# Performance work log

Hardware: AMD Instinct MI355X
Metric: run time of the kernel (lower is better)

Reference implementation:

```python
import jax, jax.numpy as jnp
import numpy as np


def setup_inputs() -> dict:
    key = jax.random.key(0)
    k0, k1, k2, k3 = jax.random.split(key, 4)
    N, C, H, W, s = 2, 16, 96, 96, 2
    x = jax.random.normal(k0, (N, C, H, W), dtype=jnp.float32)
    pos_mat = jax.random.uniform(k1, (1, H * s * W * s, 3), dtype=jnp.float32)
    mask = jnp.ones((1, 1, H * s, W * s), dtype=bool)
    w1 = jax.random.normal(k2, (3, 256), dtype=jnp.float32) * 0.1
    b1 = jnp.zeros((256,), dtype=jnp.float32)
    w2 = jax.random.normal(k3, (256, 9 * C * C), dtype=jnp.float32) * 0.02
    b2 = jnp.zeros((9 * C * C,), dtype=jnp.float32)
    return {"x": x, "pos_mat": pos_mat, "mask": mask, "w1": w1, "b1": b1,
            "w2": w2, "b2": b2, "r": 2, "hr0": H * s, "hr1": W * s}


def _unfold3x3(x):
    # torch F.unfold(x, kernel_size=3, padding=1) -> [N, C*9, H*W],
    # channel ordering: c slowest, then (kh, kw).
    N, C, H, W = x.shape
    xp = jnp.pad(x, ((0, 0), (0, 0), (1, 1), (1, 1)))
    patches = jnp.stack([xp[:, :, i:i + H, j:j + W]
                         for i in range(3) for j in range(3)], axis=2)  # [N,C,9,H,W]
    return patches.reshape(N, C * 9, H * W)


def reference(x, pos_mat, mask, w1, b1, w2, b2, r, hr0, hr1):
    s = int(np.ceil(r))  # scale_int
    N, C, H, W = x.shape

    # Pos2Weight hypernetwork: Linear(3,256) -> LeakyReLU(0.2) -> Linear(256, 9*C*C)
    p = pos_mat.reshape(-1, 3)                       # [H*s*W*s, 3]
    h = p @ w1 + b1
    h = jnp.where(h >= 0, h, 0.2 * h)
    lw = h @ w2 + b2                                 # [H*s*W*s, 9*C*C]

    # local_weight -> (s^2, H*W, 9C, C)
    lw = lw.reshape(H, s, W, s, 9 * C, C).transpose(1, 3, 0, 2, 4, 5)
    lw = lw.reshape(s * s, H * W, 9 * C, C)

    # repeat_x tiles x s^2 times along batch; all copies are identical, so the
    # unfold of up_x equals the unfold of x broadcast over the s^2 axis.
    cols = _unfold3x3(x).transpose(0, 2, 1)          # [N, H*W, 9C]

    # per-pixel batched matmul: (N,1,HW,1,9C) @ (s^2,HW,9C,C)
    out = jnp.einsum('npk,qpkc->nqpc', cols, lw)     # [N, s^2, H*W, C]

    # (N,s,s,H,W,C) -> (N,C,H,s,W,s) -> (N,C,sH,sW)
    out = out.reshape(N, s, s, H, W, C).transpose(0, 5, 3, 1, 4, 2)
    out = out.reshape(N, C, s * H, s * W)

    # masked_select with an all-True broadcast mask followed by reshape to
    # (N, C, hr0, hr1); with integer scale, hr == (sH, sW) and this is identity.
    re_sr = jnp.reshape(out, (N, C, hr0, hr1))
    return re_sr
```

## Files before the change

kernel.cpp:

```cpp
#include <hip/hip_runtime.h>
#include <stdint.h>

typedef __attribute__((ext_vector_type(8))) short          s16x8;
typedef __attribute__((ext_vector_type(8))) unsigned short u16x8;
typedef __attribute__((ext_vector_type(4))) float          f32x4;

#define HWPIX 9216
#define OSTR  68
#define ABLK  10240

static __device__ __forceinline__ unsigned short f2bf(float f) {
  unsigned int u = __float_as_uint(f);
  u += 0x7fffu + ((u >> 16) & 1u);
  return (unsigned short)(u >> 16);
}

__global__ __launch_bounds__(256)
void ml_prep(const float* __restrict__ x, const float* __restrict__ w2,
             const float* __restrict__ b2,
             unsigned short* __restrict__ Afrag, unsigned short* __restrict__ Bfrag)
{
  int idx = blockIdx.x * 256 + threadIdx.x;
  if (idx < 368640) {
    int bx = idx / 1280, r = idx - bx * 1280;
    int ks = r >> 8, mi = (r >> 6) & 3, lane = r & 63;
    int row = bx * 64 + mi * 16 + (lane & 15);
    int p = row >> 1, n2 = row & 1;
    int hh = p / 96, ww = p - hh * 96;
    int k0 = ks * 32 + (lane >> 4) * 8;
    u16x8 v;
#pragma unroll
    for (int t = 0; t < 8; t++) {
      int k = k0 + t;
      float xv = 0.f;
      if (k < 144) {
        int cc = k / 9, kidx = k - cc * 9;
        int ih = hh + kidx / 3 - 1, iw = ww + (kidx % 3) - 1;
        if (ih >= 0 && ih < 96 && iw >= 0 && iw < 96)
          xv = x[((n2 * 16 + cc) * 96 + ih) * 96 + iw];
      }
      v[t] = f2bf(xv);
    }
    *(u16x8*)(Afrag + (size_t)idx * 8) = v;
    return;
  }
  idx -= 368640;
  if (idx < 87040) {
    int lane = idx & 63;
    int u  = idx >> 6;
    int ni = u & 3;
    int u2 = u >> 2;
    int wid = u2 & 3;
    int u3 = u2 >> 2;
    int ks = u3 % 5;
    int jb = u3 / 5;
    int col = jb * 256 + wid * 64 + ni * 16 + (lane & 15);
    int k0 = ks * 32 + (lane >> 4) * 8;
    u16x8 v;
    if (col < 4096) {
      int j = col >> 4, c = col & 15;
#pragma unroll
      for (int t = 0; t < 8; t++) {
        int k = k0 + t;
        v[t] = (k < 144) ? f2bf(w2[j * 2304 + k * 16 + c]) : (unsigned short)0;
      }
    } else {
      int m = col - 4096;
      int jl = m >> 4, c = m & 15;
#pragma unroll
      for (int t = 0; t < 8; t++) {
        int k = k0 + t;
        v[t] = (jl == 0 && k < 144) ? f2bf(b2[k * 16 + c]) : (unsigned short)0;
      }
    }
    *(u16x8*)(Bfrag + (size_t)idx * 8) = v;
  }
}

struct SmemT {
  unsigned short A[ABLK];
  float hbuf[2][2][32 * OSTR];
};

__global__ __launch_bounds__(512, 2)
void ml_main(const unsigned short* __restrict__ Afrag,
             const unsigned short* __restrict__ Bfrag,
             const float* __restrict__ pos, const float* __restrict__ w1,
             const float* __restrict__ b1,
             float* __restrict__ out)
{
  __shared__ SmemT sm;
  const int tid  = threadIdx.x;
  const int lane = tid & 63;
  const int wid  = tid >> 6;
  const int wni  = wid & 3;
  const int wjb  = wid >> 2;
  const int bx   = blockIdx.x;
  const int p0   = bx * 32;

  const unsigned short* bwv = Bfrag + wni * 2048 + lane * 8;

  const unsigned short* Ablk = Afrag + (size_t)bx * ABLK;
  u16x8 av[3];
#pragma unroll
  for (int i = 0; i < 3; i++) {
    int aid = i * 512 + tid;
    if (aid < 1280) av[i] = *(const u16x8*)(Ablk + aid * 8);
  }

  float pv[4][3];
  {
    int p = p0 + (tid >> 4);
    int hh = p / 96, ww = p - hh * 96;
#pragma unroll
    for (int q = 0; q < 4; q++) {
      int m = hh * 384 + (q >> 1) * 192 + ww * 2 + (q & 1);
      pv[q][0] = pos[m * 3 + 0];
      pv[q][1] = pos[m * 3 + 1];
      pv[q][2] = pos[m * 3 + 2];
    }
  }

#pragma unroll
  for (int i = 0; i < 3; i++) {
    int aid = i * 512 + tid;
    if (aid < 1280) *(u16x8*)(sm.A + aid * 8) = av[i];
  }

  s16x8 br0[4], br1[4];
  {
    const unsigned short* bb = bwv + wjb * 5 * 8192;
#pragma unroll
    for (int ni = 0; ni < 4; ni++)
      br0[ni] = *(const s16x8*)(bb + ni * 512);
  }

  f32x4 oa[4][4];
#pragma unroll
  for (int mi = 0; mi < 4; mi++)
#pragma unroll
    for (int reg = 0; reg < 4; reg++) {
      f32x4 z = {0.f, 0.f, 0.f, 0.f};
      oa[mi][reg] = z;
    }

  __syncthreads();

  auto step = [&](int s, s16x8 (&bx0)[4], s16x8 (&bx1)[4]) {
    {
      int p_h = tid >> 4, jl = tid & 15;
#pragma unroll
      for (int wj = 0; wj < 2; wj++) {
        int jb = 2 * s + wj;
        if (jb <= 16) {
          f32x4 hv;
          if (jb < 16) {
            int j = jb * 16 + jl;
            float wa = w1[j], wb = w1[256 + j], wc = w1[512 + j], bb = b1[j];
#pragma unroll
            for (int q = 0; q < 4; q++) {
              float h = pv[q][0] * wa + pv[q][1] * wb + pv[q][2] * wc + bb;
              hv[q] = (h >= 0.f) ? h : 0.2f * h;
            }
          } else {
            float v = (jl == 0) ? 1.f : 0.f;
            hv[0] = v; hv[1] = v; hv[2] = v; hv[3] = v;
          }
          *(f32x4*)&sm.hbuf[s & 1][wj][p_h * OSTR + jl * 4] = hv;
        }
      }
    }
    __syncthreads();

    const int jb_w = 2 * s + wjb;
    if (jb_w <= 16) {
      f32x4 acc[4][4];
#pragma unroll
      for (int mi = 0; mi < 4; mi++)
#pragma unroll
        for (int ni = 0; ni < 4; ni++) {
          f32x4 z = {0.f, 0.f, 0.f, 0.f};
          acc[mi][ni] = z;
        }

#pragma unroll
      for (int ks = 0; ks < 5; ks++) {
        s16x8 (&bcur)[4]  = (ks & 1) ? bx1 : bx0;
        s16x8 (&bnext)[4] = (ks & 1) ? bx0 : bx1;
        if (ks < 4 || jb_w + 2 <= 16) {
          int njb = (ks < 4) ? jb_w : jb_w + 2;
          int nks = (ks < 4) ? ks + 1 : 0;
          const unsigned short* bb = bwv + (njb * 5 + nks) * 8192;
#pragma unroll
          for (int ni = 0; ni < 4; ni++)
            bnext[ni] = *(const s16x8*)(bb + ni * 512);
        }
        s16x8 af[4];
#pragma unroll
        for (int mi = 0; mi < 4; mi++)
          af[mi] = *(const s16x8*)(sm.A + (ks * 4 + mi) * 512 + lane * 8);
#pragma unroll
        for (int mi = 0; mi < 4; mi++)
#pragma unroll
          for (int ni = 0; ni < 4; ni++)
            acc[mi][ni] = __builtin_amdgcn_mfma_f32_16x16x32_bf16(af[mi], bcur[ni], acc[mi][ni], 0, 0, 0);
      }

      const float* hb = &sm.hbuf[s & 1][wjb][0];
#pragma unroll
      for (int mi = 0; mi < 4; mi++) {
        int pb = mi * 8 + (lane >> 4) * 2;
#pragma unroll
        for (int ni = 0; ni < 4; ni++) {
          int jl = wni * 4 + ni;
          const float* hp = &hb[pb * OSTR + jl * 4];
          f32x4 h0 = *(const f32x4*)hp;
          f32x4 h1 = *(const f32x4*)(hp + OSTR);
          f32x4 a = acc[mi][ni];
          oa[mi][0] += h0 * a[0];
          oa[mi][1] += h0 * a[1];
          oa[mi][2] += h1 * a[2];
          oa[mi][3] += h1 * a[3];
        }
      }
    }
  };

#pragma unroll 1
  for (int s2 = 0; s2 < 4; s2++) {
    step(2 * s2,     br0, br1);
    step(2 * s2 + 1, br1, br0);
  }
  step(8, br0, br1);

  float* outr  = (float*)sm.A;
  float* outr2 = (float*)&sm.hbuf[0][0][0];
  __syncthreads();
  if (wid == 0 || wid == 4) {
    float* dst = (wid == 0) ? outr : outr2;
#pragma unroll
    for (int mi = 0; mi < 4; mi++)
#pragma unroll
      for (int reg = 0; reg < 4; reg++) {
        int row = mi * 16 + (lane >> 4) * 4 + reg;
        *(f32x4*)&dst[row * OSTR + (lane & 15) * 4] = oa[mi][reg];
      }
  }
  __syncthreads();
#pragma unroll 1
  for (int r = 1; r < 4; r++) {
    if (wid == r || wid == r + 4) {
      float* dst = (wid == r) ? outr : outr2;
#pragma unroll
      for (int mi = 0; mi < 4; mi++)
#pragma unroll
        for (int reg = 0; reg < 4; reg++) {
          int row = mi * 16 + (lane >> 4) * 4 + reg;
          f32x4* d = (f32x4*)&dst[row * OSTR + (lane & 15) * 4];
          *d += oa[mi][reg];
        }
    }
    __syncthreads();
  }

  const int hh0 = bx / 3;
  const int ww0 = (bx - hh0 * 3) * 32;
#pragma unroll 1
  for (int i = 0; i < 8; i++) {
    int flat = i * 512 + tid;
    int xl = flat & 63;
    int si = (flat >> 6) & 1;
    int c  = (flat >> 7) & 15;
    int n2 = flat >> 11;
    int pl = xl >> 1, sj = xl & 1;
    int q = si * 2 + sj;
    int row = pl * 2 + n2;
    int idx = row * OSTR + c * 4 + q;
    float v = outr[idx] + outr2[idx];
    out[((n2 * 16 + c) * 192 + hh0 * 2 + si) * 192 + ww0 * 2 + xl] = v;
  }
}

extern "C" void kernel_launch(void* const* d_in, const int* in_sizes, int n_in,
                              void* d_out, int out_size, void* d_ws, size_t ws_size,
                              hipStream_t stream) {
  const float* x   = (const float*)d_in[0];
  const float* pos = (const float*)d_in[1];
  const float* w1  = (const float*)d_in[3];
  const float* b1  = (const float*)d_in[4];
  const float* w2  = (const float*)d_in[5];
  const float* b2  = (const float*)d_in[6];
  float* out = (float*)d_out;

  unsigned short* Afrag = (unsigned short*)d_ws;
  unsigned short* Bfrag = Afrag + (size_t)288 * ABLK;

  ml_prep<<<1780, 256, 0, stream>>>(x, w2, b2, Afrag, Bfrag);
  ml_main<<<288, 512, 0, stream>>>(Afrag, Bfrag, pos, w1, b1, out);
}
```

Baseline: 84.13 us.

## Retile main kernel to 36 pixels per block over 256 blocks with swizzled LDS A

Changes each block from 32 to 36 pixels (72 GEMM rows padded to 80, 5 M-fragments), so the grid becomes 256 blocks, matching the CU count for a single wave. The prep kernel pads A fragments with zero rows, and a second set of position values covers pixels 32..35 for the hidden-layer buffer. It also XOR-swizzles the A fragment layout in shared memory to reduce bank conflicts. In exchange it adds padded MFMA work (80 rows, only 72 used), more registers per thread that may hurt the 2-blocks occupancy, and output stores that no longer cover contiguous row segments.

```diff
diff --git a/kernel.cpp b/kernel.cpp
--- a/kernel.cpp
+++ b/kernel.cpp
@@ -7,7 +7,7 @@
 
 #define HWPIX 9216
 #define OSTR  68
-#define ABLK  10240
+#define ABLK  12800
 
 static __device__ __forceinline__ unsigned short f2bf(float f) {
   unsigned int u = __float_as_uint(f);
@@ -21,30 +21,37 @@
              unsigned short* __restrict__ Afrag, unsigned short* __restrict__ Bfrag)
 {
   int idx = blockIdx.x * 256 + threadIdx.x;
-  if (idx < 368640) {
-    int bx = idx / 1280, r = idx - bx * 1280;
-    int ks = r >> 8, mi = (r >> 6) & 3, lane = r & 63;
-    int row = bx * 64 + mi * 16 + (lane & 15);
-    int p = row >> 1, n2 = row & 1;
-    int hh = p / 96, ww = p - hh * 96;
-    int k0 = ks * 32 + (lane >> 4) * 8;
+  if (idx < 409600) {
+    int bx = idx / 1600, r = idx - bx * 1600;
+    int ks = r / 320, r2 = r - ks * 320;
+    int mi = r2 >> 6, lane = r2 & 63;
+    int rowloc = mi * 16 + (lane & 15);
     u16x8 v;
-#pragma unroll
-    for (int t = 0; t < 8; t++) {
-      int k = k0 + t;
-      float xv = 0.f;
-      if (k < 144) {
-        int cc = k / 9, kidx = k - cc * 9;
-        int ih = hh + kidx / 3 - 1, iw = ww + (kidx % 3) - 1;
-        if (ih >= 0 && ih < 96 && iw >= 0 && iw < 96)
-          xv = x[((n2 * 16 + cc) * 96 + ih) * 96 + iw];
-      }
-      v[t] = f2bf(xv);
+    if (rowloc < 72) {
+      int g = bx * 72 + rowloc;
+      int p = g >> 1, n2 = g & 1;
+      int hh = p / 96, ww = p - hh * 96;
+      int k0 = ks * 32 + (lane >> 4) * 8;
+#pragma unroll
+      for (int t = 0; t < 8; t++) {
+        int k = k0 + t;
+        float xv = 0.f;
+        if (k < 144) {
+          int cc = k / 9, kidx = k - cc * 9;
+          int ih = hh + kidx / 3 - 1, iw = ww + (kidx % 3) - 1;
+          if (ih >= 0 && ih < 96 && iw >= 0 && iw < 96)
+            xv = x[((n2 * 16 + cc) * 96 + ih) * 96 + iw];
+        }
+        v[t] = f2bf(xv);
+      }
+    } else {
+#pragma unroll
+      for (int t = 0; t < 8; t++) v[t] = 0;
     }
     *(u16x8*)(Afrag + (size_t)idx * 8) = v;
     return;
   }
-  idx -= 368640;
+  idx -= 409600;
   if (idx < 87040) {
     int lane = idx & 63;
     int u  = idx >> 6;
@@ -79,7 +86,7 @@
 
 struct SmemT {
   unsigned short A[ABLK];
-  float hbuf[2][2][32 * OSTR];
+  float hbuf[2][2][40 * OSTR];
 };
 
 __global__ __launch_bounds__(512, 2)
@@ -96,21 +103,24 @@
   const int wni  = wid & 3;
   const int wjb  = wid >> 2;
   const int bx   = blockIdx.x;
-  const int p0   = bx * 32;
+  const int p0   = bx * 36;
 
   const unsigned short* bwv = Bfrag + wni * 2048 + lane * 8;
 
+  const int aswz = 8 * (lane ^ (lane >> 3));
+
   const unsigned short* Ablk = Afrag + (size_t)bx * ABLK;
-  u16x8 av[3];
-#pragma unroll
-  for (int i = 0; i < 3; i++) {
+  u16x8 av[4];
+#pragma unroll
+  for (int i = 0; i < 4; i++) {
     int aid = i * 512 + tid;
-    if (aid < 1280) av[i] = *(const u16x8*)(Ablk + aid * 8);
-  }
-
-  float pv[4][3];
+    if (aid < 1600) av[i] = *(const u16x8*)(Ablk + aid * 8);
+  }
+
+  float pv[4][3], pv2[4][3];
   {
     int p = p0 + (tid >> 4);
+    if (p > 9215) p = 9215;
     int hh = p / 96, ww = p - hh * 96;
 #pragma unroll
     for (int q = 0; q < 4; q++) {
@@ -119,12 +129,25 @@
       pv[q][1] = pos[m * 3 + 1];
       pv[q][2] = pos[m * 3 + 2];
     }
-  }
-
-#pragma unroll
-  for (int i = 0; i < 3; i++) {
+    int p2 = p0 + (tid >> 4) + 32;
+    if (p2 > 9215) p2 = 9215;
+    int hh2 = p2 / 96, ww2 = p2 - hh2 * 96;
+#pragma unroll
+    for (int q = 0; q < 4; q++) {
+      int m = hh2 * 384 + (q >> 1) * 192 + ww2 * 2 + (q & 1);
+      pv2[q][0] = pos[m * 3 + 0];
+      pv2[q][1] = pos[m * 3 + 1];
+      pv2[q][2] = pos[m * 3 + 2];
+    }
+  }
+
+#pragma unroll
+  for (int i = 0; i < 4; i++) {
     int aid = i * 512 + tid;
-    if (aid < 1280) *(u16x8*)(sm.A + aid * 8) = av[i];
+    if (aid < 1600) {
+      int unit = aid >> 6, l = aid & 63;
+      *(u16x8*)(sm.A + unit * 512 + 8 * (l ^ (l >> 3))) = av[i];
+    }
   }
 
   s16x8 br0[4], br1[4];
@@ -135,9 +158,9 @@
       br0[ni] = *(const s16x8*)(bb + ni * 512);
   }
 
-  f32x4 oa[4][4];
-#pragma unroll
-  for (int mi = 0; mi < 4; mi++)
+  f32x4 oa[5][4];
+#pragma unroll
+  for (int mi = 0; mi < 5; mi++)
 #pragma unroll
     for (int reg = 0; reg < 4; reg++) {
       f32x4 z = {0.f, 0.f, 0.f, 0.f};
@@ -153,6 +176,7 @@
       for (int wj = 0; wj < 2; wj++) {
         int jb = 2 * s + wj;
         if (jb <= 16) {
+          float* hb = &sm.hbuf[s & 1][wj][0];
           f32x4 hv;
           if (jb < 16) {
             int j = jb * 16 + jl;
@@ -162,11 +186,21 @@
               float h = pv[q][0] * wa + pv[q][1] * wb + pv[q][2] * wc + bb;
               hv[q] = (h >= 0.f) ? h : 0.2f * h;
             }
+            *(f32x4*)&hb[p_h * OSTR + jl * 4] = hv;
+            if (tid < 128) {
+#pragma unroll
+              for (int q = 0; q < 4; q++) {
+                float h = pv2[q][0] * wa + pv2[q][1] * wb + pv2[q][2] * wc + bb;
+                hv[q] = (h >= 0.f) ? h : 0.2f * h;
+              }
+              *(f32x4*)&hb[(p_h + 32) * OSTR + jl * 4] = hv;
+            }
           } else {
             float v = (jl == 0) ? 1.f : 0.f;
             hv[0] = v; hv[1] = v; hv[2] = v; hv[3] = v;
+            *(f32x4*)&hb[p_h * OSTR + jl * 4] = hv;
+            if (tid < 128) *(f32x4*)&hb[(p_h + 32) * OSTR + jl * 4] = hv;
           }
-          *(f32x4*)&sm.hbuf[s & 1][wj][p_h * OSTR + jl * 4] = hv;
         }
       }
     }
@@ -174,9 +208,9 @@
 
     const int jb_w = 2 * s + wjb;
     if (jb_w <= 16) {
-      f32x4 acc[4][4];
-#pragma unroll
-      for (int mi = 0; mi < 4; mi++)
+      f32x4 acc[5][4];
+#pragma unroll
+      for (int mi = 0; mi < 5; mi++)
 #pragma unroll
         for (int ni = 0; ni < 4; ni++) {
           f32x4 z = {0.f, 0.f, 0.f, 0.f};
@@ -195,12 +229,12 @@
           for (int ni = 0; ni < 4; ni++)
             bnext[ni] = *(const s16x8*)(bb + ni * 512);
         }
-        s16x8 af[4];
-#pragma unroll
-        for (int mi = 0; mi < 4; mi++)
-          af[mi] = *(const s16x8*)(sm.A + (ks * 4 + mi) * 512 + lane * 8);
-#pragma unroll
-        for (int mi = 0; mi < 4; mi++)
+        s16x8 af[5];
+#pragma unroll
+        for (int mi = 0; mi < 5; mi++)
+          af[mi] = *(const s16x8*)(sm.A + (ks * 5 + mi) * 512 + aswz);
+#pragma unroll
+        for (int mi = 0; mi < 5; mi++)
 #pragma unroll
           for (int ni = 0; ni < 4; ni++)
             acc[mi][ni] = __builtin_amdgcn_mfma_f32_16x16x32_bf16(af[mi], bcur[ni], acc[mi][ni], 0, 0, 0);
@@ -208,7 +242,7 @@
 
       const float* hb = &sm.hbuf[s & 1][wjb][0];
 #pragma unroll
-      for (int mi = 0; mi < 4; mi++) {
+      for (int mi = 0; mi < 5; mi++) {
         int pb = mi * 8 + (lane >> 4) * 2;
 #pragma unroll
         for (int ni = 0; ni < 4; ni++) {
@@ -239,7 +273,7 @@
   if (wid == 0 || wid == 4) {
     float* dst = (wid == 0) ? outr : outr2;
 #pragma unroll
-    for (int mi = 0; mi < 4; mi++)
+    for (int mi = 0; mi < 5; mi++)
 #pragma unroll
       for (int reg = 0; reg < 4; reg++) {
         int row = mi * 16 + (lane >> 4) * 4 + reg;
@@ -252,7 +286,7 @@
     if (wid == r || wid == r + 4) {
       float* dst = (wid == r) ? outr : outr2;
 #pragma unroll
-      for (int mi = 0; mi < 4; mi++)
+      for (int mi = 0; mi < 5; mi++)
 #pragma unroll
         for (int reg = 0; reg < 4; reg++) {
           int row = mi * 16 + (lane >> 4) * 4 + reg;
@@ -263,21 +297,21 @@
     __syncthreads();
   }
 
-  const int hh0 = bx / 3;
-  const int ww0 = (bx - hh0 * 3) * 32;
 #pragma unroll 1
-  for (int i = 0; i < 8; i++) {
+  for (int i = 0; i < 9; i++) {
     int flat = i * 512 + tid;
-    int xl = flat & 63;
-    int si = (flat >> 6) & 1;
-    int c  = (flat >> 7) & 15;
-    int n2 = flat >> 11;
-    int pl = xl >> 1, sj = xl & 1;
+    int inner = flat % 72, outer = flat / 72;
+    int p_l = inner >> 1, sj = inner & 1;
+    int si = outer & 1;
+    int c  = (outer >> 1) & 15;
+    int n2 = outer >> 5;
     int q = si * 2 + sj;
-    int row = pl * 2 + n2;
+    int row = p_l * 2 + n2;
     int idx = row * OSTR + c * 4 + q;
     float v = outr[idx] + outr2[idx];
-    out[((n2 * 16 + c) * 192 + hh0 * 2 + si) * 192 + ww0 * 2 + xl] = v;
+    int p = p0 + p_l;
+    int hh = p / 96, ww = p - hh * 96;
+    out[((n2 * 16 + c) * 192 + hh * 2 + si) * 192 + ww * 2 + sj] = v;
   }
 }
 
@@ -293,8 +327,8 @@
   float* out = (float*)d_out;
 
   unsigned short* Afrag = (unsigned short*)d_ws;
-  unsigned short* Bfrag = Afrag + (size_t)288 * ABLK;
-
-  ml_prep<<<1780, 256, 0, stream>>>(x, w2, b2, Afrag, Bfrag);
-  ml_main<<<288, 512, 0, stream>>>(Afrag, Bfrag, pos, w1, b1, out);
+  unsigned short* Bfrag = Afrag + (size_t)256 * ABLK;
+
+  ml_prep<<<1940, 256, 0, stream>>>(x, w2, b2, Afrag, Bfrag);
+  ml_main<<<256, 512, 0, stream>>>(Afrag, Bfrag, pos, w1, b1, out);
 }
```

Result: slower. 192.2 us (+128.4%).
